# Kernel tuning notes

Hardware: AMD Instinct MI355X
Metric: run time of the kernel (lower is better)

The kernel has to match this reference:

```python
import jax, jax.numpy as jnp
import numpy as np


def setup_inputs() -> dict:
    key = jax.random.key(0)
    ks = jax.random.split(key, 8)
    B, C, H, W = 4, 256, 64, 64
    Cqk = C // 8
    s = 1.0 / np.sqrt(C)
    return {
        "x": jax.random.normal(ks[0], (B, C, H, W), jnp.float32),
        "wq": jax.random.normal(ks[1], (Cqk, C), jnp.float32) * s,
        "bq": jax.random.normal(ks[2], (Cqk,), jnp.float32) * 0.01,
        "wk": jax.random.normal(ks[3], (Cqk, C), jnp.float32) * s,
        "bk": jax.random.normal(ks[4], (Cqk,), jnp.float32) * 0.01,
        "wv": jax.random.normal(ks[5], (C, C), jnp.float32) * s,
        "bv": jax.random.normal(ks[6], (C,), jnp.float32) * 0.01,
        "gamma": jax.random.normal(ks[7], (1,), jnp.float32),
    }


def reference(x, wq, bq, wk, bk, wv, bv, gamma):
    B, C, H, W = x.shape
    N = H * W
    xf = x.reshape(B, C, N)  # [B, C, N]
    # 1x1 convs are per-pixel channel matmuls
    q = jnp.einsum('oc,bcn->bon', wq, xf) + bq[None, :, None]  # [B, C//8, N]
    k = jnp.einsum('oc,bcn->bon', wk, xf) + bk[None, :, None]  # [B, C//8, N]
    v = jnp.einsum('oc,bcn->bon', wv, xf) + bv[None, :, None]  # [B, C, N]
    # energy[b, n, m] = q[b,:,n] . k[b,:,m]  (unscaled)
    energy = jnp.einsum('bcn,bcm->bnm', q, k)  # [B, N, N]
    # original applies softmax over dim=-2, i.e. over the query index n per column m
    attn = jax.nn.softmax(energy, axis=-2)  # [B, N, N]
    at_map = jnp.transpose(attn, (0, 2, 1))  # returned map, [B, N, N]
    # sa_map = V @ attn : bmm([B,C,N],[B,N,N]) -> [B,C,N]
    sa = jnp.einsum('bcn,bnm->bcm', v, attn).reshape(B, C, H, W)
    out = x + gamma[0] * sa
    return (out, at_map)
```

## Files before the change

kernel.cpp:

```cpp
#include <hip/hip_runtime.h>
#include <hip/hip_bf16.h>
#include <cstdint>
#include <cstddef>

#define NPIX 4096
#define CIN  256
#define CQK  32
#define BSZ  4

typedef __attribute__((ext_vector_type(8))) short          bf16x8;
typedef __attribute__((ext_vector_type(4))) float          f32x4;
typedef __attribute__((ext_vector_type(8))) unsigned short u16x8;

static __device__ inline unsigned short f2bf(float f) {
    __hip_bfloat16 h = __float2bfloat16(f);
    unsigned short u;
    __builtin_memcpy(&u, &h, 2);
    return u;
}

static __device__ inline void gl2lds16(const void* g, void* l) {
    __builtin_amdgcn_global_load_lds(
        (const __attribute__((address_space(1))) unsigned int*)g,
        (__attribute__((address_space(3))) unsigned int*)l,
        16, 0, 0);
}

__global__ __launch_bounds__(256) void proj_kernel(
    const float* __restrict__ x, const float* __restrict__ W,
    const float* __restrict__ bias, float* __restrict__ y, int Cout)
{
    __shared__ float Wl[8][CIN];
    const int t  = threadIdx.x;
    const int n0 = blockIdx.x * 1024;
    const int o0 = blockIdx.y * 8;
    const int b  = blockIdx.z;

    #pragma unroll
    for (int j = 0; j < 8; ++j) {
        int flat = t + 256 * j;
        int row = flat >> 8, col = flat & 255;
        Wl[row][col] = W[(o0 + row) * CIN + col];
    }
    __syncthreads();

    float acc[8][4];
    #pragma unroll
    for (int o = 0; o < 8; ++o)
        #pragma unroll
        for (int i = 0; i < 4; ++i) acc[o][i] = 0.f;

    const float* xb = x + ((size_t)b * CIN) * NPIX + n0 + t * 4;
    #pragma unroll 4
    for (int c = 0; c < CIN; ++c) {
        float4 xv = *(const float4*)(xb + (size_t)c * NPIX);
        #pragma unroll
        for (int o = 0; o < 8; ++o) {
            float w = Wl[o][c];
            acc[o][0] = fmaf(w, xv.x, acc[o][0]);
            acc[o][1] = fmaf(w, xv.y, acc[o][1]);
            acc[o][2] = fmaf(w, xv.z, acc[o][2]);
            acc[o][3] = fmaf(w, xv.w, acc[o][3]);
        }
    }
    #pragma unroll
    for (int o = 0; o < 8; ++o) {
        float bb = bias[o0 + o];
        float4 r = { acc[o][0] + bb, acc[o][1] + bb,
                     acc[o][2] + bb, acc[o][3] + bb };
        *(float4*)(y + ((size_t)(b * Cout + o0 + o)) * NPIX + n0 + t * 4) = r;
    }
}

__global__ __launch_bounds__(256) void proj_qk_kernel(
    const float* __restrict__ x,
    const float* __restrict__ wq, const float* __restrict__ bq,
    const float* __restrict__ wk, const float* __restrict__ bk,
    float* __restrict__ qout, float* __restrict__ kout)
{
    __shared__ float Wl[CIN][12];
    const int t  = threadIdx.x;
    const int n0 = blockIdx.x * 512;
    const int og = blockIdx.y * 8;
    const int b  = blockIdx.z;
    const bool isK = og >= CQK;
    const float* W    = isK ? wk : wq;
    const float* bias = isK ? bk : bq;
    float* y          = isK ? kout : qout;
    const int o0      = isK ? og - CQK : og;

    #pragma unroll
    for (int j = 0; j < 8; ++j) {
        int flat = t + 256 * j;
        int o = flat >> 8, c = flat & 255;
        Wl[c][o] = W[(o0 + o) * CIN + c];
    }
    __syncthreads();

    float acc[8][2];
    #pragma unroll
    for (int o = 0; o < 8; ++o) { acc[o][0] = 0.f; acc[o][1] = 0.f; }

    const float* xb = x + ((size_t)b * CIN) * NPIX + n0 + t * 2;
    #pragma unroll 4
    for (int c = 0; c < CIN; ++c) {
        float2 xv = *(const float2*)(xb + (size_t)c * NPIX);
        f32x4 w0 = *(const f32x4*)&Wl[c][0];
        f32x4 w1 = *(const f32x4*)&Wl[c][4];
        float wv[8] = { w0[0], w0[1], w0[2], w0[3],
                        w1[0], w1[1], w1[2], w1[3] };
        #pragma unroll
        for (int o = 0; o < 8; ++o) {
            acc[o][0] = fmaf(wv[o], xv.x, acc[o][0]);
            acc[o][1] = fmaf(wv[o], xv.y, acc[o][1]);
        }
    }
    #pragma unroll
    for (int o = 0; o < 8; ++o) {
        float bb = bias[o0 + o];
        float2 r = { acc[o][0] + bb, acc[o][1] + bb };
        *(float2*)(y + ((size_t)(b * CQK + o0 + o)) * NPIX + n0 + t * 2) = r;
    }
}

__global__ __launch_bounds__(256) void proj_v_bf16_kernel(
    const float* __restrict__ x, const float* __restrict__ W,
    const float* __restrict__ bias, unsigned short* __restrict__ y)
{
    __shared__ float Wl[CIN][20];
    const int t  = threadIdx.x;
    const int n0 = blockIdx.x * 512;
    const int o0 = blockIdx.y * 16;
    const int b  = blockIdx.z;

    #pragma unroll
    for (int j = 0; j < 16; ++j) {
        int flat = t + 256 * j;
        int o = flat >> 8, c = flat & 255;
        Wl[c][o] = W[(o0 + o) * CIN + c];
    }
    __syncthreads();

    float acc[16][2];
    #pragma unroll
    for (int o = 0; o < 16; ++o) { acc[o][0] = 0.f; acc[o][1] = 0.f; }

    const float* xb = x + ((size_t)b * CIN) * NPIX + n0 + t * 2;
    #pragma unroll 2
    for (int c = 0; c < CIN; ++c) {
        float2 xv = *(const float2*)(xb + (size_t)c * NPIX);
        f32x4 w0 = *(const f32x4*)&Wl[c][0];
        f32x4 w1 = *(const f32x4*)&Wl[c][4];
        f32x4 w2 = *(const f32x4*)&Wl[c][8];
        f32x4 w3 = *(const f32x4*)&Wl[c][12];
        float wv[16] = { w0[0], w0[1], w0[2], w0[3],
                         w1[0], w1[1], w1[2], w1[3],
                         w2[0], w2[1], w2[2], w2[3],
                         w3[0], w3[1], w3[2], w3[3] };
        #pragma unroll
        for (int o = 0; o < 16; ++o) {
            acc[o][0] = fmaf(wv[o], xv.x, acc[o][0]);
            acc[o][1] = fmaf(wv[o], xv.y, acc[o][1]);
        }
    }
    #pragma unroll
    for (int o = 0; o < 16; ++o) {
        float bb = bias[o0 + o];
        ushort2 r;
        r.x = f2bf(acc[o][0] + bb);
        r.y = f2bf(acc[o][1] + bb);
        *(ushort2*)(y + ((size_t)(b * CIN + o0 + o)) * NPIX + n0 + t * 2) = r;
    }
}

__global__ __launch_bounds__(512) void energy_softmax_kernel(
    const float* __restrict__ q, const float* __restrict__ k,
    float* __restrict__ at_map, unsigned short* __restrict__ attn_bf)
{
    __shared__ float kk[CQK][12];
    __shared__ float wredM[8][8];
    __shared__ float wredS[8][8];
    const int t  = threadIdx.x;
    const int m0 = blockIdx.x * 8;
    const int b  = blockIdx.y;
    const int lane = t & 63, wid = t >> 6;

    if (t < 256) {
        int c = t >> 3, mi = t & 7;
        kk[c][mi] = k[((size_t)(b * CQK + c)) * NPIX + m0 + mi];
    }
    __syncthreads();

    float s[8][8];
    #pragma unroll
    for (int mi = 0; mi < 8; ++mi)
        #pragma unroll
        for (int i = 0; i < 8; ++i) s[mi][i] = 0.f;

    const float* qb = q + ((size_t)b * CQK) * NPIX + t * 8;
    #pragma unroll 2
    for (int c = 0; c < CQK; ++c) {
        float4 q0 = *(const float4*)(qb + (size_t)c * NPIX);
        float4 q1 = *(const float4*)(qb + (size_t)c * NPIX + 4);
        f32x4 k0 = *(const f32x4*)&kk[c][0];
        f32x4 k1 = *(const f32x4*)&kk[c][4];
        float kv[8] = { k0[0], k0[1], k0[2], k0[3],
                        k1[0], k1[1], k1[2], k1[3] };
        #pragma unroll
        for (int mi = 0; mi < 8; ++mi) {
            float w = kv[mi];
            s[mi][0] = fmaf(w, q0.x, s[mi][0]);
            s[mi][1] = fmaf(w, q0.y, s[mi][1]);
            s[mi][2] = fmaf(w, q0.z, s[mi][2]);
            s[mi][3] = fmaf(w, q0.w, s[mi][3]);
            s[mi][4] = fmaf(w, q1.x, s[mi][4]);
            s[mi][5] = fmaf(w, q1.y, s[mi][5]);
            s[mi][6] = fmaf(w, q1.z, s[mi][6]);
            s[mi][7] = fmaf(w, q1.w, s[mi][7]);
        }
    }

    #pragma unroll
    for (int mi = 0; mi < 8; ++mi) {
        float mx = s[mi][0];
        #pragma unroll
        for (int i = 1; i < 8; ++i) mx = fmaxf(mx, s[mi][i]);
        #pragma unroll
        for (int off = 1; off < 64; off <<= 1)
            mx = fmaxf(mx, __shfl_xor(mx, off, 64));
        if (lane == 0) wredM[mi][wid] = mx;
    }
    __syncthreads();

    #pragma unroll
    for (int mi = 0; mi < 8; ++mi) {
        float bmx = wredM[mi][0];
        #pragma unroll
        for (int w = 1; w < 8; ++w) bmx = fmaxf(bmx, wredM[mi][w]);
        float sum = 0.f;
        #pragma unroll
        for (int i = 0; i < 8; ++i) {
            s[mi][i] = __expf(s[mi][i] - bmx);
            sum += s[mi][i];
        }
        #pragma unroll
        for (int off = 1; off < 64; off <<= 1)
            sum += __shfl_xor(sum, off, 64);
        if (lane == 0) wredS[mi][wid] = sum;
    }
    __syncthreads();

    #pragma unroll
    for (int mi = 0; mi < 8; ++mi) {
        float bsum = 0.f;
        #pragma unroll
        for (int w = 0; w < 8; ++w) bsum += wredS[mi][w];
        float inv = 1.f / bsum;
        size_t rowoff = ((size_t)(b * NPIX) + m0 + mi) * NPIX + t * 8;
        float a0 = s[mi][0]*inv, a1 = s[mi][1]*inv, a2 = s[mi][2]*inv, a3 = s[mi][3]*inv;
        float a4 = s[mi][4]*inv, a5 = s[mi][5]*inv, a6 = s[mi][6]*inv, a7 = s[mi][7]*inv;
        f32x4 r0 = { a0, a1, a2, a3 };
        f32x4 r1 = { a4, a5, a6, a7 };
        __builtin_nontemporal_store(r0, (f32x4*)(at_map + rowoff));
        __builtin_nontemporal_store(r1, (f32x4*)(at_map + rowoff + 4));
        if (attn_bf) {
            u16x8 rb;
            rb[0] = f2bf(a0); rb[1] = f2bf(a1); rb[2] = f2bf(a2); rb[3] = f2bf(a3);
            rb[4] = f2bf(a4); rb[5] = f2bf(a5); rb[6] = f2bf(a6); rb[7] = f2bf(a7);
            *(u16x8*)(attn_bf + rowoff) = rb;
        }
    }
}

__global__ __launch_bounds__(256) void sa_gemm_mfma(
    const unsigned short* __restrict__ v,
    const unsigned short* __restrict__ attn,
    const float* __restrict__ x, const float* __restrict__ gptr,
    float* __restrict__ out)
{
    __shared__ __align__(16) unsigned short As[128 * 64];
    __shared__ __align__(16) unsigned short Bs[64 * 64];

    const int t = threadIdx.x, lane = t & 63, w = t >> 6;
    const int m_base = blockIdx.x * 64;
    const int c_base = blockIdx.y * 128;
    const int b      = blockIdx.z;
    const int wc = (w >> 1) * 64, wm = (w & 1) * 32;

    const int lrow = lane >> 3;
    const int glog = (lane & 7) ^ lrow;
    const unsigned short* aSrc[4];
    const unsigned short* bSrc[2];
    #pragma unroll
    for (int qi = 0; qi < 4; ++qi)
        aSrc[qi] = v    + ((size_t)(b * CIN + c_base + w * 32 + qi * 8 + lrow)) * NPIX + glog * 8;
    #pragma unroll
    for (int qi = 0; qi < 2; ++qi)
        bSrc[qi] = attn + ((size_t)b * NPIX + m_base + w * 16 + qi * 8 + lrow) * NPIX + glog * 8;

    const int l15 = lane & 15, q4 = lane >> 4;
    const int x0 = (q4 ^ (lane & 7)) * 8;
    const int x1 = ((q4 ^ 4) ^ (lane & 7)) * 8;
    const int baseA = (wc + l15) * 64;
    const int baseB = (wm + l15) * 64;

    f32x4 acc[4][2];
    #pragma unroll
    for (int i = 0; i < 4; ++i)
        #pragma unroll
        for (int j = 0; j < 2; ++j) acc[i][j] = (f32x4)(0.0f);

    for (int k0 = 0; k0 < NPIX; k0 += 64) {
        #pragma unroll
        for (int qi = 0; qi < 4; ++qi)
            gl2lds16(aSrc[qi] + k0, &As[(w * 32 + qi * 8) * 64]);
        #pragma unroll
        for (int qi = 0; qi < 2; ++qi)
            gl2lds16(bSrc[qi] + k0, &Bs[(w * 16 + qi * 8) * 64]);
        __syncthreads();
        #pragma unroll
        for (int ks = 0; ks < 2; ++ks) {
            const int xo = ks ? x1 : x0;
            bf16x8 af[4], bfr[2];
            #pragma unroll
            for (int i = 0; i < 4; ++i)
                af[i] = *(const bf16x8*)&As[baseA + i * 1024 + xo];
            #pragma unroll
            for (int j = 0; j < 2; ++j)
                bfr[j] = *(const bf16x8*)&Bs[baseB + j * 1024 + xo];
            #pragma unroll
            for (int i = 0; i < 4; ++i)
                #pragma unroll
                for (int j = 0; j < 2; ++j)
                    acc[i][j] = __builtin_amdgcn_mfma_f32_16x16x32_bf16(
                        af[i], bfr[j], acc[i][j], 0, 0, 0);
        }
        __syncthreads();
    }

    const float g = gptr[0];
    #pragma unroll
    for (int i = 0; i < 4; ++i) {
        int c = c_base + wc + i * 16 + q4 * 4;
        #pragma unroll
        for (int j = 0; j < 2; ++j) {
            int m = m_base + wm + j * 16 + l15;
            #pragma unroll
            for (int r = 0; r < 4; ++r) {
                size_t idx = ((size_t)(b * CIN + c + r)) * NPIX + m;
                float val = x[idx] + g * acc[i][j][r];
                __builtin_nontemporal_store(val, &out[idx]);
            }
        }
    }
}

__global__ __launch_bounds__(256) void sa_gemm_kernel(
    const float* __restrict__ v, const float* __restrict__ at_map,
    const float* __restrict__ x, const float* __restrict__ gptr,
    float* __restrict__ out)
{
    __shared__ float Vt[32][68];
    __shared__ float At[32][68];
    const int t  = threadIdx.x;
    const int m0 = blockIdx.x * 64;
    const int c0 = blockIdx.y * 64;
    const int b  = blockIdx.z;
    const int r  = t >> 2, qd = t & 3;
    const int tc = t & 15, tm = t >> 4;

    const float* vb = v      + ((size_t)(b * CIN  + c0 + r)) * NPIX + qd * 4;
    const float* ab = at_map + ((size_t)(b * NPIX + m0 + r)) * NPIX + qd * 4;

    float acc[4][4];
    #pragma unroll
    for (int i = 0; i < 4; ++i)
        #pragma unroll
        for (int j = 0; j < 4; ++j) acc[i][j] = 0.f;

    for (int n0 = 0; n0 < NPIX; n0 += 32) {
        float4 v0 = *(const float4*)(vb + n0);
        float4 v1 = *(const float4*)(vb + n0 + 16);
        float4 a0 = *(const float4*)(ab + n0);
        float4 a1 = *(const float4*)(ab + n0 + 16);
        Vt[qd*4+0][r] = v0.x; Vt[qd*4+1][r] = v0.y;
        Vt[qd*4+2][r] = v0.z; Vt[qd*4+3][r] = v0.w;
        Vt[16+qd*4+0][r] = v1.x; Vt[16+qd*4+1][r] = v1.y;
        Vt[16+qd*4+2][r] = v1.z; Vt[16+qd*4+3][r] = v1.w;
        At[qd*4+0][r] = a0.x; At[qd*4+1][r] = a0.y;
        At[qd*4+2][r] = a0.z; At[qd*4+3][r] = a0.w;
        At[16+qd*4+0][r] = a1.x; At[16+qd*4+1][r] = a1.y;
        At[16+qd*4+2][r] = a1.z; At[16+qd*4+3][r] = a1.w;
        __syncthreads();
        #pragma unroll
        for (int kk = 0; kk < 32; ++kk) {
            float4 a  = *(const float4*)&Vt[kk][tc * 4];
            float4 bb = *(const float4*)&At[kk][tm * 4];
            acc[0][0] = fmaf(a.x, bb.x, acc[0][0]);
            acc[0][1] = fmaf(a.x, bb.y, acc[0][1]);
            acc[0][2] = fmaf(a.x, bb.z, acc[0][2]);
            acc[0][3] = fmaf(a.x, bb.w, acc[0][3]);
            acc[1][0] = fmaf(a.y, bb.x, acc[1][0]);
            acc[1][1] = fmaf(a.y, bb.y, acc[1][1]);
            acc[1][2] = fmaf(a.y, bb.z, acc[1][2]);
            acc[1][3] = fmaf(a.y, bb.w, acc[1][3]);
            acc[2][0] = fmaf(a.z, bb.x, acc[2][0]);
            acc[2][1] = fmaf(a.z, bb.y, acc[2][1]);
            acc[2][2] = fmaf(a.z, bb.z, acc[2][2]);
            acc[2][3] = fmaf(a.z, bb.w, acc[2][3]);
            acc[3][0] = fmaf(a.w, bb.x, acc[3][0]);
            acc[3][1] = fmaf(a.w, bb.y, acc[3][1]);
            acc[3][2] = fmaf(a.w, bb.z, acc[3][2]);
            acc[3][3] = fmaf(a.w, bb.w, acc[3][3]);
        }
        __syncthreads();
    }

    const float g = *gptr;
    #pragma unroll
    for (int i = 0; i < 4; ++i) {
        size_t row = ((size_t)(b * CIN + c0 + tc * 4 + i)) * NPIX + m0 + tm * 4;
        float4 xv = *(const float4*)(x + row);
        float4 o  = { xv.x + g * acc[i][0], xv.y + g * acc[i][1],
                      xv.z + g * acc[i][2], xv.w + g * acc[i][3] };
        *(float4*)(out + row) = o;
    }
}

extern "C" void kernel_launch(void* const* d_in, const int* in_sizes, int n_in,
                              void* d_out, int out_size, void* d_ws, size_t ws_size,
                              hipStream_t stream) {
    const float* x     = (const float*)d_in[0];
    const float* wq    = (const float*)d_in[1];
    const float* bq    = (const float*)d_in[2];
    const float* wk    = (const float*)d_in[3];
    const float* bk    = (const float*)d_in[4];
    const float* wv    = (const float*)d_in[5];
    const float* bv    = (const float*)d_in[6];
    const float* gamma = (const float*)d_in[7];

    float* out    = (float*)d_out;
    float* at_map = out + (size_t)BSZ * CIN * NPIX;

    const size_t qk_elems  = (size_t)BSZ * CQK * NPIX;
    const size_t v_elems   = (size_t)BSZ * CIN * NPIX;
    const size_t nn_elems  = (size_t)BSZ * NPIX * NPIX;

    const size_t need_fast = 2 * qk_elems * 4 + v_elems * 2 + nn_elems * 2;

    if (ws_size >= need_fast) {
        float*          q       = (float*)d_ws;
        float*          k       = q + qk_elems;
        unsigned short* v_bf    = (unsigned short*)(k + qk_elems);
        unsigned short* attn_bf = v_bf + v_elems;

        proj_qk_kernel<<<dim3(NPIX/512, 8, BSZ), 256, 0, stream>>>(
            x, wq, bq, wk, bk, q, k);
        proj_v_bf16_kernel<<<dim3(NPIX/512, CIN/16, BSZ), 256, 0, stream>>>(
            x, wv, bv, v_bf);

        energy_softmax_kernel<<<dim3(NPIX/8, BSZ), 512, 0, stream>>>(q, k, at_map, attn_bf);

        sa_gemm_mfma<<<dim3(NPIX/64, CIN/128, BSZ), 256, 0, stream>>>(
            v_bf, attn_bf, x, gamma, out);
    } else {
        float* q = (float*)d_ws;
        float* k = q + qk_elems;
        float* v = k + qk_elems;

        proj_kernel<<<dim3(NPIX/1024, CQK/8, BSZ), 256, 0, stream>>>(x, wq, bq, q, CQK);
        proj_kernel<<<dim3(NPIX/1024, CQK/8, BSZ), 256, 0, stream>>>(x, wk, bk, k, CQK);
        proj_kernel<<<dim3(NPIX/1024, CIN/8, BSZ), 256, 0, stream>>>(x, wv, bv, v, CIN);

        energy_softmax_kernel<<<dim3(NPIX/8, BSZ), 512, 0, stream>>>(q, k, at_map, nullptr);

        sa_gemm_kernel<<<dim3(NPIX/64, CIN/64, BSZ), 256, 0, stream>>>(
            v, at_map, x, gamma, out);
    }
}
```

Measured before the change: 566.2 us.

## Defer softmax normalization to GEMM epilogue and remap GEMM blocks across XCDs

The energy kernel now writes the unnormalized exponentials to the bf16 attention buffer before the block-wide sum reduction, and stores the per-column inverse sums in a small new buffer. The MFMA GEMM applies that inverse as a per-column scale in its epilogue. This lets the bf16 store overlap the reduction and keeps the multiply off the critical path. The GEMM grid is flattened to a 1D launch with an XCD-aware mapping, so blocks sharing attention rows land on the same die's L2. The non-temporal stores are replaced by plain stores.

Measured after the change: 539.7 us. 4.7% less time.

```diff
diff --git a/kernel.cpp b/kernel.cpp
--- a/kernel.cpp
+++ b/kernel.cpp
@@ -175,7 +175,8 @@
 
 __global__ __launch_bounds__(512) void energy_softmax_kernel(
     const float* __restrict__ q, const float* __restrict__ k,
-    float* __restrict__ at_map, unsigned short* __restrict__ attn_bf)
+    float* __restrict__ at_map, unsigned short* __restrict__ attn_bf,
+    float* __restrict__ inv_buf)
 {
     __shared__ float kk[CQK][12];
     __shared__ float wredM[8][8];
@@ -243,6 +244,13 @@
             s[mi][i] = __expf(s[mi][i] - bmx);
             sum += s[mi][i];
         }
+        if (attn_bf) {
+            size_t rowoff = ((size_t)(b * NPIX) + m0 + mi) * NPIX + t * 8;
+            u16x8 rb;
+            #pragma unroll
+            for (int i = 0; i < 8; ++i) rb[i] = f2bf(s[mi][i]);
+            *(u16x8*)(attn_bf + rowoff) = rb;
+        }
         #pragma unroll
         for (int off = 1; off < 64; off <<= 1)
             sum += __shfl_xor(sum, off, 64);
@@ -256,19 +264,12 @@
         #pragma unroll
         for (int w = 0; w < 8; ++w) bsum += wredS[mi][w];
         float inv = 1.f / bsum;
+        if (inv_buf && t == mi) inv_buf[(size_t)b * NPIX + m0 + mi] = inv;
         size_t rowoff = ((size_t)(b * NPIX) + m0 + mi) * NPIX + t * 8;
-        float a0 = s[mi][0]*inv, a1 = s[mi][1]*inv, a2 = s[mi][2]*inv, a3 = s[mi][3]*inv;
-        float a4 = s[mi][4]*inv, a5 = s[mi][5]*inv, a6 = s[mi][6]*inv, a7 = s[mi][7]*inv;
-        f32x4 r0 = { a0, a1, a2, a3 };
-        f32x4 r1 = { a4, a5, a6, a7 };
-        __builtin_nontemporal_store(r0, (f32x4*)(at_map + rowoff));
-        __builtin_nontemporal_store(r1, (f32x4*)(at_map + rowoff + 4));
-        if (attn_bf) {
-            u16x8 rb;
-            rb[0] = f2bf(a0); rb[1] = f2bf(a1); rb[2] = f2bf(a2); rb[3] = f2bf(a3);
-            rb[4] = f2bf(a4); rb[5] = f2bf(a5); rb[6] = f2bf(a6); rb[7] = f2bf(a7);
-            *(u16x8*)(attn_bf + rowoff) = rb;
-        }
+        float4 r0 = { s[mi][0]*inv, s[mi][1]*inv, s[mi][2]*inv, s[mi][3]*inv };
+        float4 r1 = { s[mi][4]*inv, s[mi][5]*inv, s[mi][6]*inv, s[mi][7]*inv };
+        *(float4*)(at_map + rowoff)     = r0;
+        *(float4*)(at_map + rowoff + 4) = r1;
     }
 }
 
@@ -276,15 +277,22 @@
     const unsigned short* __restrict__ v,
     const unsigned short* __restrict__ attn,
     const float* __restrict__ x, const float* __restrict__ gptr,
+    const float* __restrict__ inv_buf,
     float* __restrict__ out)
 {
     __shared__ __align__(16) unsigned short As[128 * 64];
     __shared__ __align__(16) unsigned short Bs[64 * 64];
 
     const int t = threadIdx.x, lane = t & 63, w = t >> 6;
-    const int m_base = blockIdx.x * 64;
-    const int c_base = blockIdx.y * 128;
-    const int b      = blockIdx.z;
+
+    const int gid  = blockIdx.x;
+    const int xcd  = gid & 7;
+    const int slot = gid >> 3;
+    const int c_t     = slot & 1;
+    const int m_local = (slot >> 1) & 7;
+    const int b       = slot >> 4;
+    const int m_base = (xcd * 8 + m_local) * 64;
+    const int c_base = c_t * 128;
     const int wc = (w >> 1) * 64, wm = (w & 1) * 32;
 
     const int lrow = lane >> 3;
@@ -339,17 +347,21 @@
     }
 
     const float g = gptr[0];
+    float invm[2];
+    #pragma unroll
+    for (int j = 0; j < 2; ++j)
+        invm[j] = inv_buf[(size_t)b * NPIX + m_base + wm + j * 16 + l15];
     #pragma unroll
     for (int i = 0; i < 4; ++i) {
         int c = c_base + wc + i * 16 + q4 * 4;
         #pragma unroll
         for (int j = 0; j < 2; ++j) {
             int m = m_base + wm + j * 16 + l15;
+            float gi = g * invm[j];
             #pragma unroll
             for (int r = 0; r < 4; ++r) {
                 size_t idx = ((size_t)(b * CIN + c + r)) * NPIX + m;
-                float val = x[idx] + g * acc[i][j][r];
-                __builtin_nontemporal_store(val, &out[idx]);
+                out[idx] = x[idx] + gi * acc[i][j][r];
             }
         }
     }
@@ -445,24 +457,28 @@
     const size_t qk_elems  = (size_t)BSZ * CQK * NPIX;
     const size_t v_elems   = (size_t)BSZ * CIN * NPIX;
     const size_t nn_elems  = (size_t)BSZ * NPIX * NPIX;
-
-    const size_t need_fast = 2 * qk_elems * 4 + v_elems * 2 + nn_elems * 2;
+    const size_t inv_elems = (size_t)BSZ * NPIX;
+
+    const size_t need_fast = 2 * qk_elems * 4 + v_elems * 2 + nn_elems * 2
+                           + inv_elems * 4;
 
     if (ws_size >= need_fast) {
         float*          q       = (float*)d_ws;
         float*          k       = q + qk_elems;
         unsigned short* v_bf    = (unsigned short*)(k + qk_elems);
         unsigned short* attn_bf = v_bf + v_elems;
+        float*          inv_buf = (float*)(attn_bf + nn_elems);
 
         proj_qk_kernel<<<dim3(NPIX/512, 8, BSZ), 256, 0, stream>>>(
             x, wq, bq, wk, bk, q, k);
         proj_v_bf16_kernel<<<dim3(NPIX/512, CIN/16, BSZ), 256, 0, stream>>>(
             x, wv, bv, v_bf);
 
-        energy_softmax_kernel<<<dim3(NPIX/8, BSZ), 512, 0, stream>>>(q, k, at_map, attn_bf);
-
-        sa_gemm_mfma<<<dim3(NPIX/64, CIN/128, BSZ), 256, 0, stream>>>(
-            v_bf, attn_bf, x, gamma, out);
+        energy_softmax_kernel<<<dim3(NPIX/8, BSZ), 512, 0, stream>>>(
+            q, k, at_map, attn_bf, inv_buf);
+
+        sa_gemm_mfma<<<dim3(512, 1, 1), 256, 0, stream>>>(
+            v_bf, attn_bf, x, gamma, inv_buf, out);
     } else {
         float* q = (float*)d_ws;
         float* k = q + qk_elems;
@@ -472,7 +488,8 @@
         proj_kernel<<<dim3(NPIX/1024, CQK/8, BSZ), 256, 0, stream>>>(x, wk, bk, k, CQK);
         proj_kernel<<<dim3(NPIX/1024, CIN/8, BSZ), 256, 0, stream>>>(x, wv, bv, v, CIN);
 
-        energy_softmax_kernel<<<dim3(NPIX/8, BSZ), 512, 0, stream>>>(q, k, at_map, nullptr);
+        energy_softmax_kernel<<<dim3(NPIX/8, BSZ), 512, 0, stream>>>(
+            q, k, at_map, nullptr, nullptr);
 
         sa_gemm_kernel<<<dim3(NPIX/64, CIN/64, BSZ), 256, 0, stream>>>(
             v, at_map, x, gamma, out);
```

## Fuse energy, column softmax and V@attn into one two-pass MFMA kernel

Applied to the files above, without the earlier changes.

Replaces the separate energy/softmax kernel and the bf16 attention GEMM with one fused kernel. It first computes online max/sum statistics per column, then recomputes the energies with MFMA, writes the normalized fp32 map and feeds bf16 probabilities through LDS into the V@P MFMA. Q and K are stored transposed as split hi/lo bf16 pairs so the QK product stays near fp32 accuracy. This removes the 128MB bf16 attention intermediate round trip and one launch, at the cost of computing the energies twice and a fixed XCD-aware grid mapping.

Result: faster. 506.4 us (-10.6%).

```diff
diff --git a/kernel.cpp b/kernel.cpp
--- a/kernel.cpp
+++ b/kernel.cpp
@@ -7,6 +7,9 @@
 #define CIN  256
 #define CQK  32
 #define BSZ  4
+#define MT   32
+#define NT   64
+#define PSW  72
 
 typedef __attribute__((ext_vector_type(8))) short          bf16x8;
 typedef __attribute__((ext_vector_type(4))) float          f32x4;
@@ -17,6 +20,13 @@
     unsigned short u;
     __builtin_memcpy(&u, &h, 2);
     return u;
+}
+
+static __device__ inline float bf2f(unsigned short u) {
+    unsigned int x = ((unsigned int)u) << 16;
+    float f;
+    __builtin_memcpy(&f, &x, 4);
+    return f;
 }
 
 static __device__ inline void gl2lds16(const void* g, void* l) {
@@ -72,11 +82,11 @@
     }
 }
 
-__global__ __launch_bounds__(256) void proj_qk_kernel(
+__global__ __launch_bounds__(256) void proj_qk_t_kernel(
     const float* __restrict__ x,
     const float* __restrict__ wq, const float* __restrict__ bq,
     const float* __restrict__ wk, const float* __restrict__ bk,
-    float* __restrict__ qout, float* __restrict__ kout)
+    unsigned short* __restrict__ qt, unsigned short* __restrict__ kt)
 {
     __shared__ float Wl[CIN][12];
     const int t  = threadIdx.x;
@@ -86,7 +96,7 @@
     const bool isK = og >= CQK;
     const float* W    = isK ? wk : wq;
     const float* bias = isK ? bk : bq;
-    float* y          = isK ? kout : qout;
+    unsigned short* y = (isK ? kt : qt) + ((size_t)b * NPIX) * 64;
     const int o0      = isK ? og - CQK : og;
 
     #pragma unroll
@@ -116,10 +126,18 @@
         }
     }
     #pragma unroll
-    for (int o = 0; o < 8; ++o) {
-        float bb = bias[o0 + o];
-        float2 r = { acc[o][0] + bb, acc[o][1] + bb };
-        *(float2*)(y + ((size_t)(b * CQK + o0 + o)) * NPIX + n0 + t * 2) = r;
+    for (int i = 0; i < 2; ++i) {
+        size_t n = (size_t)(n0 + t * 2 + i);
+        u16x8 hi, lo;
+        #pragma unroll
+        for (int o = 0; o < 8; ++o) {
+            float val = acc[o][i] + bias[o0 + o];
+            unsigned short h = f2bf(val);
+            hi[o] = h;
+            lo[o] = f2bf(val - bf2f(h));
+        }
+        *(u16x8*)(y + n * 64 + o0)      = hi;
+        *(u16x8*)(y + n * 64 + 32 + o0) = lo;
     }
 }
 
@@ -175,7 +193,7 @@
 
 __global__ __launch_bounds__(512) void energy_softmax_kernel(
     const float* __restrict__ q, const float* __restrict__ k,
-    float* __restrict__ at_map, unsigned short* __restrict__ attn_bf)
+    float* __restrict__ at_map)
 {
     __shared__ float kk[CQK][12];
     __shared__ float wredM[8][8];
@@ -257,99 +275,157 @@
         for (int w = 0; w < 8; ++w) bsum += wredS[mi][w];
         float inv = 1.f / bsum;
         size_t rowoff = ((size_t)(b * NPIX) + m0 + mi) * NPIX + t * 8;
-        float a0 = s[mi][0]*inv, a1 = s[mi][1]*inv, a2 = s[mi][2]*inv, a3 = s[mi][3]*inv;
-        float a4 = s[mi][4]*inv, a5 = s[mi][5]*inv, a6 = s[mi][6]*inv, a7 = s[mi][7]*inv;
-        f32x4 r0 = { a0, a1, a2, a3 };
-        f32x4 r1 = { a4, a5, a6, a7 };
-        __builtin_nontemporal_store(r0, (f32x4*)(at_map + rowoff));
-        __builtin_nontemporal_store(r1, (f32x4*)(at_map + rowoff + 4));
-        if (attn_bf) {
-            u16x8 rb;
-            rb[0] = f2bf(a0); rb[1] = f2bf(a1); rb[2] = f2bf(a2); rb[3] = f2bf(a3);
-            rb[4] = f2bf(a4); rb[5] = f2bf(a5); rb[6] = f2bf(a6); rb[7] = f2bf(a7);
-            *(u16x8*)(attn_bf + rowoff) = rb;
-        }
-    }
-}
-
-__global__ __launch_bounds__(256) void sa_gemm_mfma(
+        float4 r0 = { s[mi][0]*inv, s[mi][1]*inv, s[mi][2]*inv, s[mi][3]*inv };
+        float4 r1 = { s[mi][4]*inv, s[mi][5]*inv, s[mi][6]*inv, s[mi][7]*inv };
+        *(float4*)(at_map + rowoff)     = r0;
+        *(float4*)(at_map + rowoff + 4) = r1;
+    }
+}
+
+__global__ __launch_bounds__(512, 4) void fused_attn_mfma(
+    const unsigned short* __restrict__ qt,
+    const unsigned short* __restrict__ kt,
     const unsigned short* __restrict__ v,
-    const unsigned short* __restrict__ attn,
     const float* __restrict__ x, const float* __restrict__ gptr,
-    float* __restrict__ out)
+    float* __restrict__ at_map, float* __restrict__ out)
 {
-    __shared__ __align__(16) unsigned short As[128 * 64];
-    __shared__ __align__(16) unsigned short Bs[64 * 64];
+    __shared__ __align__(16) unsigned short Vs[CIN * NT];
+    __shared__ __align__(16) unsigned short Ps[MT * PSW];
+    __shared__ float MSred[2][4][16][2];
+    __shared__ float IvS[MT];
 
     const int t = threadIdx.x, lane = t & 63, w = t >> 6;
-    const int m_base = blockIdx.x * 64;
-    const int c_base = blockIdx.y * 128;
-    const int b      = blockIdx.z;
-    const int wc = (w >> 1) * 64, wm = (w & 1) * 32;
-
+    const int gid = blockIdx.x;
+    const int xcd = gid & 7, slot = gid >> 3;
+    const int b  = xcd & 3;
+    const int m0 = (slot + ((xcd >> 2) << 6)) * MT;
+
+    const int l15 = lane & 15, q4 = lane >> 4;
+    const int msub = w >> 2, nsub = w & 3;
+    const int wc = w * 32;
     const int lrow = lane >> 3;
     const int glog = (lane & 7) ^ lrow;
-    const unsigned short* aSrc[4];
-    const unsigned short* bSrc[2];
-    #pragma unroll
-    for (int qi = 0; qi < 4; ++qi)
-        aSrc[qi] = v    + ((size_t)(b * CIN + c_base + w * 32 + qi * 8 + lrow)) * NPIX + glog * 8;
-    #pragma unroll
-    for (int qi = 0; qi < 2; ++qi)
-        bSrc[qi] = attn + ((size_t)b * NPIX + m_base + w * 16 + qi * 8 + lrow) * NPIX + glog * 8;
-
-    const int l15 = lane & 15, q4 = lane >> 4;
-    const int x0 = (q4 ^ (lane & 7)) * 8;
-    const int x1 = ((q4 ^ 4) ^ (lane & 7)) * 8;
-    const int baseA = (wc + l15) * 64;
-    const int baseB = (wm + l15) * 64;
-
-    f32x4 acc[4][2];
-    #pragma unroll
-    for (int i = 0; i < 4; ++i)
-        #pragma unroll
-        for (int j = 0; j < 2; ++j) acc[i][j] = (f32x4)(0.0f);
-
-    for (int k0 = 0; k0 < NPIX; k0 += 64) {
+
+    const unsigned short* kp =
+        kt + ((size_t)(b * NPIX + m0 + msub * 16 + l15)) * 64 + q4 * 8;
+    const bf16x8 khi = *(const bf16x8*)kp;
+    const bf16x8 klo = *(const bf16x8*)(kp + 32);
+
+    const unsigned short* qp =
+        qt + ((size_t)(b * NPIX) + nsub * 16 + l15) * 64 + q4 * 8;
+
+    const unsigned short* vbase = v + (size_t)b * CIN * NPIX;
+
+    float M = -1e30f, S = 0.f;
+    bf16x8 qh = *(const bf16x8*)qp;
+    bf16x8 ql = *(const bf16x8*)(qp + 32);
+    for (int tile = 0; tile < NPIX / NT; ++tile) {
+        bf16x8 qh2 = qh, ql2 = ql;
+        if (tile + 1 < NPIX / NT) {
+            const unsigned short* p = qp + (size_t)(tile + 1) * (NT * 64);
+            qh2 = *(const bf16x8*)p;
+            ql2 = *(const bf16x8*)(p + 32);
+        }
+        f32x4 s4 = (f32x4)(0.0f);
+        s4 = __builtin_amdgcn_mfma_f32_16x16x32_bf16(qh, khi, s4, 0, 0, 0);
+        s4 = __builtin_amdgcn_mfma_f32_16x16x32_bf16(ql, khi, s4, 0, 0, 0);
+        s4 = __builtin_amdgcn_mfma_f32_16x16x32_bf16(qh, klo, s4, 0, 0, 0);
+        float mx = fmaxf(fmaxf(s4[0], s4[1]), fmaxf(s4[2], s4[3]));
+        if (mx > M) { S *= __expf(M - mx); M = mx; }
+        S += __expf(s4[0] - M); S += __expf(s4[1] - M);
+        S += __expf(s4[2] - M); S += __expf(s4[3] - M);
+        qh = qh2; ql = ql2;
+    }
+    #pragma unroll
+    for (int off = 16; off < 64; off <<= 1) {
+        float Mo = __shfl_xor(M, off, 64);
+        float So = __shfl_xor(S, off, 64);
+        float Mn = fmaxf(M, Mo);
+        S = S * __expf(M - Mn) + So * __expf(Mo - Mn);
+        M = Mn;
+    }
+    if (q4 == 0) {
+        MSred[msub][nsub][l15][0] = M;
+        MSred[msub][nsub][l15][1] = S;
+    }
+    __syncthreads();
+    {
+        float Mf = MSred[msub][0][l15][0], Sf = MSred[msub][0][l15][1];
+        #pragma unroll
+        for (int j = 1; j < 4; ++j) {
+            float Mo = MSred[msub][j][l15][0], So = MSred[msub][j][l15][1];
+            float Mn = fmaxf(Mf, Mo);
+            Sf = Sf * __expf(Mf - Mn) + So * __expf(Mo - Mn);
+            Mf = Mn;
+        }
+        M = Mf;
+        S = 1.0f / Sf;
+        if ((w == 0 || w == 4) && q4 == 0) IvS[msub * 16 + l15] = S;
+    }
+    __syncthreads();
+
+    f32x4 acc[2][2];
+    acc[0][0] = (f32x4)(0.0f); acc[0][1] = (f32x4)(0.0f);
+    acc[1][0] = (f32x4)(0.0f); acc[1][1] = (f32x4)(0.0f);
+
+    qh = *(const bf16x8*)qp;
+    ql = *(const bf16x8*)(qp + 32);
+
+    const size_t amrow = ((size_t)(b * NPIX + m0 + msub * 16 + l15)) * NPIX
+                       + nsub * 16 + q4 * 4;
+
+    for (int tile = 0; tile < NPIX / NT; ++tile) {
         #pragma unroll
         for (int qi = 0; qi < 4; ++qi)
-            gl2lds16(aSrc[qi] + k0, &As[(w * 32 + qi * 8) * 64]);
-        #pragma unroll
-        for (int qi = 0; qi < 2; ++qi)
-            gl2lds16(bSrc[qi] + k0, &Bs[(w * 16 + qi * 8) * 64]);
+            gl2lds16(vbase + (size_t)(wc + qi * 8 + lrow) * NPIX + tile * NT + glog * 8,
+                     &Vs[(wc + qi * 8) * NT]);
+        bf16x8 qh2 = qh, ql2 = ql;
+        if (tile + 1 < NPIX / NT) {
+            const unsigned short* p = qp + (size_t)(tile + 1) * (NT * 64);
+            qh2 = *(const bf16x8*)p;
+            ql2 = *(const bf16x8*)(p + 32);
+        }
+        f32x4 s4 = (f32x4)(0.0f);
+        s4 = __builtin_amdgcn_mfma_f32_16x16x32_bf16(qh, khi, s4, 0, 0, 0);
+        s4 = __builtin_amdgcn_mfma_f32_16x16x32_bf16(ql, khi, s4, 0, 0, 0);
+        s4 = __builtin_amdgcn_mfma_f32_16x16x32_bf16(qh, klo, s4, 0, 0, 0);
+        float p0 = __expf(s4[0] - M), p1 = __expf(s4[1] - M);
+        float p2 = __expf(s4[2] - M), p3 = __expf(s4[3] - M);
+        ushort4 up;
+        up.x = f2bf(p0); up.y = f2bf(p1); up.z = f2bf(p2); up.w = f2bf(p3);
+        *(ushort4*)&Ps[(msub * 16 + l15) * PSW + nsub * 16 + q4 * 4] = up;
         __syncthreads();
+        f32x4 an = { p0 * S, p1 * S, p2 * S, p3 * S };
+        *(f32x4*)(at_map + amrow + (size_t)tile * NT) = an;
         #pragma unroll
         for (int ks = 0; ks < 2; ++ks) {
-            const int xo = ks ? x1 : x0;
-            bf16x8 af[4], bfr[2];
-            #pragma unroll
-            for (int i = 0; i < 4; ++i)
-                af[i] = *(const bf16x8*)&As[baseA + i * 1024 + xo];
-            #pragma unroll
-            for (int j = 0; j < 2; ++j)
-                bfr[j] = *(const bf16x8*)&Bs[baseB + j * 1024 + xo];
-            #pragma unroll
-            for (int i = 0; i < 4; ++i)
-                #pragma unroll
-                for (int j = 0; j < 2; ++j)
-                    acc[i][j] = __builtin_amdgcn_mfma_f32_16x16x32_bf16(
-                        af[i], bfr[j], acc[i][j], 0, 0, 0);
+            const int pg = ((ks * 4 + q4) ^ (l15 & 7)) * 8;
+            bf16x8 a0 = *(const bf16x8*)&Vs[(wc + l15) * NT + pg];
+            bf16x8 a1 = *(const bf16x8*)&Vs[(wc + 16 + l15) * NT + pg];
+            bf16x8 b0 = *(const bf16x8*)&Ps[l15 * PSW + ks * 32 + q4 * 8];
+            bf16x8 b1 = *(const bf16x8*)&Ps[(16 + l15) * PSW + ks * 32 + q4 * 8];
+            acc[0][0] = __builtin_amdgcn_mfma_f32_16x16x32_bf16(a0, b0, acc[0][0], 0, 0, 0);
+            acc[0][1] = __builtin_amdgcn_mfma_f32_16x16x32_bf16(a0, b1, acc[0][1], 0, 0, 0);
+            acc[1][0] = __builtin_amdgcn_mfma_f32_16x16x32_bf16(a1, b0, acc[1][0], 0, 0, 0);
+            acc[1][1] = __builtin_amdgcn_mfma_f32_16x16x32_bf16(a1, b1, acc[1][1], 0, 0, 0);
         }
         __syncthreads();
+        qh = qh2; ql = ql2;
     }
 
     const float g = gptr[0];
-    #pragma unroll
-    for (int i = 0; i < 4; ++i) {
-        int c = c_base + wc + i * 16 + q4 * 4;
+    const float gi0 = g * IvS[l15], gi1 = g * IvS[16 + l15];
+    #pragma unroll
+    for (int i = 0; i < 2; ++i) {
+        int c = wc + i * 16 + q4 * 4;
         #pragma unroll
         for (int j = 0; j < 2; ++j) {
-            int m = m_base + wm + j * 16 + l15;
+            int m = m0 + j * 16 + l15;
+            float gi = j ? gi1 : gi0;
             #pragma unroll
             for (int r = 0; r < 4; ++r) {
                 size_t idx = ((size_t)(b * CIN + c + r)) * NPIX + m;
-                float val = x[idx] + g * acc[i][j][r];
-                __builtin_nontemporal_store(val, &out[idx]);
+                out[idx] = x[idx] + gi * acc[i][j][r];
             }
         }
     }
@@ -442,27 +518,24 @@
     float* out    = (float*)d_out;
     float* at_map = out + (size_t)BSZ * CIN * NPIX;
 
-    const size_t qk_elems  = (size_t)BSZ * CQK * NPIX;
-    const size_t v_elems   = (size_t)BSZ * CIN * NPIX;
-    const size_t nn_elems  = (size_t)BSZ * NPIX * NPIX;
-
-    const size_t need_fast = 2 * qk_elems * 4 + v_elems * 2 + nn_elems * 2;
+    const size_t qk_elems = (size_t)BSZ * CQK * NPIX;
+    const size_t v_elems  = (size_t)BSZ * CIN * NPIX;
+    const size_t qt_elems = (size_t)BSZ * NPIX * 64;
+
+    const size_t need_fast = qt_elems * 2 * 2 + v_elems * 2;
 
     if (ws_size >= need_fast) {
-        float*          q       = (float*)d_ws;
-        float*          k       = q + qk_elems;
-        unsigned short* v_bf    = (unsigned short*)(k + qk_elems);
-        unsigned short* attn_bf = v_bf + v_elems;
-
-        proj_qk_kernel<<<dim3(NPIX/512, 8, BSZ), 256, 0, stream>>>(
-            x, wq, bq, wk, bk, q, k);
+        unsigned short* qtp  = (unsigned short*)d_ws;
+        unsigned short* ktp  = qtp + qt_elems;
+        unsigned short* v_bf = ktp + qt_elems;
+
+        proj_qk_t_kernel<<<dim3(NPIX/512, 8, BSZ), 256, 0, stream>>>(
+            x, wq, bq, wk, bk, qtp, ktp);
         proj_v_bf16_kernel<<<dim3(NPIX/512, CIN/16, BSZ), 256, 0, stream>>>(
             x, wv, bv, v_bf);
 
-        energy_softmax_kernel<<<dim3(NPIX/8, BSZ), 512, 0, stream>>>(q, k, at_map, attn_bf);
-
-        sa_gemm_mfma<<<dim3(NPIX/64, CIN/128, BSZ), 256, 0, stream>>>(
-            v_bf, attn_bf, x, gamma, out);
+        fused_attn_mfma<<<dim3(512, 1, 1), 512, 0, stream>>>(
+            qtp, ktp, v_bf, x, gamma, at_map, out);
     } else {
         float* q = (float*)d_ws;
         float* k = q + qk_elems;
@@ -472,7 +545,7 @@
         proj_kernel<<<dim3(NPIX/1024, CQK/8, BSZ), 256, 0, stream>>>(x, wk, bk, k, CQK);
         proj_kernel<<<dim3(NPIX/1024, CIN/8, BSZ), 256, 0, stream>>>(x, wv, bv, v, CIN);
 
-        energy_softmax_kernel<<<dim3(NPIX/8, BSZ), 512, 0, stream>>>(q, k, at_map, nullptr);
+        energy_softmax_kernel<<<dim3(NPIX/8, BSZ), 512, 0, stream>>>(q, k, at_map);
 
         sa_gemm_kernel<<<dim3(NPIX/64, CIN/64, BSZ), 256, 0, stream>>>(
             v, at_map, x, gamma, out);
```
